# Kernel optimization log

Measured on AMD Instinct MI355X. Metric: run time of the kernel, lower is better.

The kernel has to match this reference:

```python
import jax, jax.numpy as jnp
import numpy as np
from jax import lax


def setup_inputs() -> dict:
    key = jax.random.key(0)
    k1, k2 = jax.random.split(key)
    x = jax.random.normal(k1, (16, 256, 64, 64), dtype=jnp.float32)
    weight = jax.random.normal(k2, (1024, 256), dtype=jnp.float32)  # codebook (K, C)
    return {"x": x, "weight": weight}


def reference(x, weight):
    B, C, H, W = x.shape
    # (b c h w) -> (b h w) c
    xf = jnp.transpose(x, (0, 2, 3, 1)).reshape(-1, C)  # [N, C]
    d = (jnp.sum(xf * xf, axis=1, keepdims=True)
         + jnp.sum(weight * weight, axis=1)
         - 2.0 * (xf @ weight.T))
    indices = jnp.argmin(d, axis=1)  # [N], int
    z = weight[indices]  # [N, C] embedding lookup
    codebook_loss = jnp.mean((z - lax.stop_gradient(xf)) ** 2)
    commitment_loss = jnp.mean((xf - lax.stop_gradient(z)) ** 2)
    # straight-through estimator
    zq = xf + lax.stop_gradient(z - xf)
    zq = zq.reshape(B, H, W, C).transpose(0, 3, 1, 2)  # back to [B, C, H, W]
    sequence = indices.reshape(B, H, W)
    return zq, sequence, codebook_loss, commitment_loss
```

## Files before the change

kernel.cpp:

```cpp
#include <hip/hip_runtime.h>
#include <cfloat>
#include <climits>

#define B_   16
#define C_   256
#define K_   1024
#define HW_  4096
#define N_   (B_ * HW_)
#define CHW_ (C_ * HW_)

#define SEQ_OFF  16777216
#define LOSS_OFF (SEQ_OFF + N_)
#define WT_F    0
#define WN_F    262144
#define WNU_F   263168
#define WQ_F    264192
#define RLIST_F 395264
#define RCNT_F  526336
#define WMAX_F  526337

#define RL_CAP  131072
#define EPS_GAP 0.1f
#define XSCL    20.0f
#define XINV    0.05f
#define XOVF    6.3f

typedef int i32x4  __attribute__((ext_vector_type(4)));
typedef int i32x16 __attribute__((ext_vector_type(16)));

__device__ __forceinline__ int pack4b(int b0, int b1, int b2, int b3) {
    return (b0 & 0xFF) | ((b1 & 0xFF) << 8) | ((b2 & 0xFF) << 16) | ((b3 & 0xFF) << 24);
}

__global__ __launch_bounds__(256) void wmax_kernel(
    const float* __restrict__ w, unsigned* __restrict__ wmax_bits)
{
    const int tid = blockIdx.x * 256 + threadIdx.x;
    float mx = 0.f;
#pragma unroll
    for (int q = 0; q < 4; ++q) {
        const float4 v = reinterpret_cast<const float4*>(w)[tid * 4 + q];
        mx = fmaxf(mx, fmaxf(fmaxf(fabsf(v.x), fabsf(v.y)), fmaxf(fabsf(v.z), fabsf(v.w))));
    }
#pragma unroll
    for (int m = 1; m < 64; m <<= 1) mx = fmaxf(mx, __shfl_xor(mx, m, 64));
    if ((threadIdx.x & 63) == 0) atomicMax(wmax_bits, __float_as_uint(mx));
}

__global__ __launch_bounds__(256) void wprep_kernel(
    const float* __restrict__ w, const unsigned* __restrict__ wmax_bits,
    unsigned char* __restrict__ wq, float* __restrict__ w_t,
    float* __restrict__ wn, int* __restrict__ wnu)
{
    const int t = threadIdx.x;
    const int l = t & 63;
    const int k = blockIdx.x * 4 + (t >> 6);
    const float wmx = __uint_as_float(*wmax_bits);
    const float s   = 127.4f / wmx;
    const float d1  = wmx / 127.4f;
    const float sl  = s * 256.0f;

    const float4 v4 = *reinterpret_cast<const float4*>(w + (size_t)k * C_ + l * 4);
    float vv[4] = {v4.x, v4.y, v4.z, v4.w};
    float s2 = vv[0]*vv[0] + vv[1]*vv[1] + vv[2]*vv[2] + vv[3]*vv[3];
#pragma unroll
    for (int m = 1; m < 64; m <<= 1) s2 += __shfl_xor(s2, m, 64);

    const int chunk = k >> 5;
    const int col   = k & 31;
#pragma unroll
    for (int q = 0; q < 4; ++q) {
        const int c = l * 4 + q;
        const float v = vv[q];
        const int qh = (int)rintf(v * s);
        const float r = fmaf((float)qh, -d1, v);
        int ql = (int)rintf(r * sl);
        ql = max(-127, min(127, ql));
        const size_t off = (size_t)chunk * 16384 + (size_t)(c >> 5) * 1024
                         + (size_t)((c >> 4) & 1) * 512 + (size_t)col * 16 + (size_t)(c & 15);
        wq[off]        = (unsigned char)(qh & 0xFF);
        wq[off + 8192] = (unsigned char)(ql & 0xFF);
        w_t[(size_t)c * K_ + k] = v;
    }
    if (l == 0) {
        wn[k] = s2;
        wnu[k] = (int)rintf(s2 * (2560.0f / d1));
    }
}

__global__ __launch_bounds__(256) void argmin_i8_kernel(
    const float* __restrict__ x, const unsigned char* __restrict__ wq,
    const int* __restrict__ wnu, const unsigned* __restrict__ wmax_bits,
    float* __restrict__ seq, int* __restrict__ rlist, int* __restrict__ rcount)
{
    __shared__ __align__(16) char lds[32768];
    const int t  = threadIdx.x;
    const int l  = t & 63;
    const int wv = t >> 6;
    const int col = l & 31;
    const int khalf = l >> 5;
    const int nb = blockIdx.x;
    const int b  = nb >> 5;
    const int hw0 = (nb & 31) << 7;
    const float* xb = x + (size_t)b * CHW_ + hw0;

    char* const buf0 = lds;
    char* const buf1 = lds + 16384;

#define STAGE32(ch, dst)                                                          \
    {                                                                             \
        _Pragma("unroll")                                                         \
        for (int rr = 0; rr < 4; ++rr) {                                          \
            const int sIdx = wv * 4 + rr;                                         \
            __builtin_amdgcn_global_load_lds(                                     \
                (const __attribute__((address_space(1))) void*)                   \
                    (wq + (size_t)(ch) * 16384 + sIdx * 1024 + l * 16),           \
                (__attribute__((address_space(3))) void*)((dst) + sIdx * 1024),   \
                16, 0, 0);                                                        \
        }                                                                         \
    }

    STAGE32(0, buf1);

    i32x4 ah8[8], al8[8];
    float mx = 0.f;
    {
        float* xs = (float*)buf0;
        const int row = wv * 32 + col;
#pragma unroll
        for (int cc = 0; cc < 8; ++cc) {
#pragma unroll
            for (int qq = 0; qq < 4; ++qq) {
                const int fi = qq * 256 + t;
                const int cl = fi >> 5;
                const int r4 = (fi & 31) << 2;
                const float4 v = *reinterpret_cast<const float4*>(
                    xb + (size_t)(cc * 32 + cl) * HW_ + r4);
                *reinterpret_cast<float4*>(xs + cl * 128 + r4) = v;
            }
            __syncthreads();
            int qh[16], ql[16];
#pragma unroll
            for (int j = 0; j < 16; ++j) {
                const float v = xs[(khalf * 16 + j) * 128 + row];
                mx = fmaxf(mx, fabsf(v));
                int h = (int)rintf(v * XSCL);
                h = max(-127, min(127, h));
                const float r = fmaf((float)h, -XINV, v);
                int lo = (int)rintf(r * (XSCL * 256.0f));
                lo = max(-127, min(127, lo));
                qh[j] = h; ql[j] = lo;
            }
            ah8[cc] = (i32x4){ pack4b(qh[0],qh[1],qh[2],qh[3]),   pack4b(qh[4],qh[5],qh[6],qh[7]),
                               pack4b(qh[8],qh[9],qh[10],qh[11]), pack4b(qh[12],qh[13],qh[14],qh[15]) };
            al8[cc] = (i32x4){ pack4b(ql[0],ql[1],ql[2],ql[3]),   pack4b(ql[4],ql[5],ql[6],ql[7]),
                               pack4b(ql[8],ql[9],ql[10],ql[11]), pack4b(ql[12],ql[13],ql[14],ql[15]) };
            __syncthreads();
        }
    }

    mx = fmaxf(mx, __shfl_xor(mx, 32, 64));
    if (khalf == 0 && mx > XOVF) {
        const int pos = atomicAdd(rcount, 1);
        if (pos < RL_CAP) rlist[pos] = b * HW_ + hw0 + wv * 32 + col;
    }

    const float wmx = __uint_as_float(*wmax_bits);
    const int eps_u = (int)(32614.4f / wmx);

    int m1p[16], m2p[16];
#pragma unroll
    for (int r = 0; r < 16; ++r) { m1p[r] = INT_MAX; m2p[r] = INT_MAX; }

    for (int ch = 0; ch < 32; ++ch) {
        char* const curbuf = (ch & 1) ? buf0 : buf1;
        if (ch < 31) STAGE32(ch + 1, (ch & 1) ? buf1 : buf0);
        const int wnu_l = wnu[ch * 32 + col];

        i32x16 aH, aX;
#pragma unroll
        for (int r = 0; r < 16; ++r) { aH[r] = 0; aX[r] = 0; }

#pragma unroll
        for (int ks = 0; ks < 8; ++ks) {
            const i32x4 bh = *reinterpret_cast<const i32x4*>(curbuf + ks * 1024 + (l << 4));
            const i32x4 bl = *reinterpret_cast<const i32x4*>(curbuf + 8192 + ks * 1024 + (l << 4));
            aH = __builtin_amdgcn_mfma_i32_32x32x32_i8(ah8[ks], bh, aH, 0, 0, 0);
            aX = __builtin_amdgcn_mfma_i32_32x32x32_i8(ah8[ks], bl, aX, 0, 0, 0);
            aX = __builtin_amdgcn_mfma_i32_32x32x32_i8(al8[ks], bh, aX, 0, 0, 0);
        }

#pragma unroll
        for (int r = 0; r < 16; ++r) {
            const int T  = (aH[r] << 8) + aX[r];
            const int D  = wnu_l - T;
            const int Dp = (D & ~31) | ch;
            m2p[r] = min(m2p[r], max(m1p[r], Dp));
            m1p[r] = min(m1p[r], Dp);
        }
        __syncthreads();
    }
#undef STAGE32

    int k1[16];
#pragma unroll
    for (int r = 0; r < 16; ++r) k1[r] = ((m1p[r] & 31) << 5) | col;
#pragma unroll
    for (int mask = 1; mask <= 16; mask <<= 1) {
#pragma unroll
        for (int r = 0; r < 16; ++r) {
            const int om1 = __shfl_xor(m1p[r], mask, 64);
            const int ok1 = __shfl_xor(k1[r],  mask, 64);
            const int om2 = __shfl_xor(m2p[r], mask, 64);
            const int nm2 = min(min(m2p[r], om2), max(m1p[r], om1));
            const bool lt = om1 < m1p[r] || (om1 == m1p[r] && ok1 < k1[r]);
            m1p[r] = lt ? om1 : m1p[r];
            k1[r]  = lt ? ok1 : k1[r];
            m2p[r] = nm2;
        }
    }

    if (col == 0) {
#pragma unroll
        for (int r = 0; r < 16; ++r) {
            const int row_local = (r & 3) + 8 * (r >> 2) + 4 * khalf;
            const int n = b * HW_ + hw0 + wv * 32 + row_local;
            seq[n] = (float)k1[r];
            if (m2p[r] - m1p[r] < eps_u) {
                const int pos = atomicAdd(rcount, 1);
                if (pos < RL_CAP) rlist[pos] = n;
            }
        }
    }
}

__global__ __launch_bounds__(256) void rescue_kernel(
    const float* __restrict__ x, const float* __restrict__ w_t,
    const float* __restrict__ wnorm, const int* __restrict__ rlist,
    const int* __restrict__ rcount, float* __restrict__ seq)
{
    __shared__ float xr[C_];
    __shared__ float bvs[4];
    __shared__ int   bis[4];
    const int t = threadIdx.x;
    const int cnt = min(*rcount, RL_CAP);
    for (int ii = blockIdx.x; ii < cnt; ii += gridDim.x) {
        const int n = rlist[ii];
        const int b = n >> 12, hw = n & 4095;
        xr[t] = x[(size_t)b * CHW_ + (size_t)t * HW_ + hw];
        __syncthreads();
        float best = FLT_MAX; int bidx = 0;
#pragma unroll
        for (int q = 0; q < 4; ++q) {
            const int k = t + q * 256;
            float acc = 0.f;
            for (int c = 0; c < C_; ++c) acc = fmaf(xr[c], w_t[(size_t)c * K_ + k], acc);
            const float d = wnorm[k] - 2.f * acc;
            if (d < best || (d == best && k < bidx)) { best = d; bidx = k; }
        }
#pragma unroll
        for (int mask = 1; mask < 64; mask <<= 1) {
            const float ov = __shfl_xor(best, mask, 64);
            const int   oi = __shfl_xor(bidx, mask, 64);
            if (ov < best || (ov == best && oi < bidx)) { best = ov; bidx = oi; }
        }
        if ((t & 63) == 0) { bvs[t >> 6] = best; bis[t >> 6] = bidx; }
        __syncthreads();
        if (t == 0) {
            float bv = bvs[0]; int bi = bis[0];
#pragma unroll
            for (int w2 = 1; w2 < 4; ++w2)
                if (bvs[w2] < bv || (bvs[w2] == bv && bis[w2] < bi)) { bv = bvs[w2]; bi = bis[w2]; }
            seq[n] = (float)bi;
        }
        __syncthreads();
    }
}

__global__ __launch_bounds__(256) void gather_kernel(
    const float* __restrict__ x, const float* __restrict__ w,
    const float* __restrict__ seqf, float* __restrict__ zq,
    double* __restrict__ loss_acc)
{
    __shared__ float ws[C_ * 64];
    const int t   = threadIdx.x;
    const int nb  = blockIdx.x;
    const int b   = nb >> 6;
    const int hw0 = (nb & 63) << 6;
    {
        const int j = t >> 2, q = t & 3;
        const int idx = (int)seqf[b * HW_ + hw0 + j];
        const float* wrow = w + (size_t)idx * C_ + q * 64;
#pragma unroll
        for (int m = 0; m < 16; ++m) {
            const float4 v = *reinterpret_cast<const float4*>(wrow + m * 4);
            const int c = q * 64 + m * 4;
            ws[(c + 0) * 64 + j] = v.x;
            ws[(c + 1) * 64 + j] = v.y;
            ws[(c + 2) * 64 + j] = v.z;
            ws[(c + 3) * 64 + j] = v.w;
        }
    }
    __syncthreads();
    const int r  = t & 63;
    const int cg = t >> 6;
    const float* xb = x  + (size_t)b * CHW_ + hw0;
    float*       zb = zq + (size_t)b * CHW_ + hw0;
    float lsum = 0.f;
#pragma unroll 4
    for (int cc = 0; cc < 64; ++cc) {
        const int c = cg * 64 + cc;
        const float xv = xb[(size_t)c * HW_ + r];
        const float d  = ws[c * 64 + r] - xv;
        zb[(size_t)c * HW_ + r] = xv + d;
        lsum += d * d;
    }
#pragma unroll
    for (int off = 32; off >= 1; off >>= 1) lsum += __shfl_down(lsum, off, 64);
    __syncthreads();
    if ((t & 63) == 0) ws[t >> 6] = lsum;
    __syncthreads();
    if (t == 0)
        atomicAdd(loss_acc, (double)(ws[0] + ws[1] + ws[2] + ws[3]));
}

__global__ void finalize_kernel(const double* __restrict__ acc, float* __restrict__ loss_out)
{
    const double s = *acc;
    const float m = (float)(s / (double)((size_t)N_ * C_));
    loss_out[0] = m;
    loss_out[1] = m;
}

extern "C" void kernel_launch(void* const* d_in, const int* in_sizes, int n_in,
                              void* d_out, int out_size, void* d_ws, size_t ws_size,
                              hipStream_t stream)
{
    (void)in_sizes; (void)n_in; (void)out_size; (void)d_ws; (void)ws_size;
    const float* x = (const float*)d_in[0];
    const float* w = (const float*)d_in[1];
    float* out = (float*)d_out;

    float*         w_t    = out + WT_F;
    float*         wn     = out + WN_F;
    int*           wnu    = (int*)(out + WNU_F);
    unsigned char* wq     = (unsigned char*)(out + WQ_F);
    int*           rlist  = (int*)(out + RLIST_F);
    int*           rcount = (int*)(out + RCNT_F);
    unsigned*      wmaxb  = (unsigned*)(out + WMAX_F);
    float*         seq    = out + SEQ_OFF;
    double*        loss_acc = (double*)(out + LOSS_OFF);

    hipMemsetAsync((void*)wmaxb, 0, 4, stream);
    hipMemsetAsync((void*)rcount, 0, 4, stream);
    wmax_kernel<<<64, 256, 0, stream>>>(w, wmaxb);
    wprep_kernel<<<256, 256, 0, stream>>>(w, wmaxb, wq, w_t, wn, wnu);
    argmin_i8_kernel<<<512, 256, 0, stream>>>(x, wq, wnu, wmaxb, seq, rlist, rcount);
    rescue_kernel<<<1024, 256, 0, stream>>>(x, w_t, wn, rlist, rcount, seq);
    hipMemsetAsync((char*)d_out + (size_t)LOSS_OFF * 4, 0, 8, stream);
    gather_kernel<<<1024, 256, 0, stream>>>(x, w, seq, out, loss_acc);
    finalize_kernel<<<1, 1, 0, stream>>>(loss_acc, out + LOSS_OFF);
}
```

Before: 206.5 us.

## Deepen codebook staging to a 4-buffer, 3-ahead pipeline with explicit vmcnt waits

Replaces double-buffered LDS staging of int8 codebook chunks with a four-slot ring that prefetches three chunks ahead. Each step waits only on the oldest outstanding load using explicit vmcnt/lgkmcnt waits and a raw s_barrier instead of __syncthreads. The wnu norms are preloaded into LDS, and MFMA sections are raised in priority with s_setprio. LDS use grows from 32KB to about 68KB per block, which may reduce how many blocks fit on a CU.

```diff
diff --git a/kernel.cpp b/kernel.cpp
--- a/kernel.cpp
+++ b/kernel.cpp
@@ -93,7 +93,7 @@
     const int* __restrict__ wnu, const unsigned* __restrict__ wmax_bits,
     float* __restrict__ seq, int* __restrict__ rlist, int* __restrict__ rcount)
 {
-    __shared__ __align__(16) char lds[32768];
+    __shared__ __align__(16) char lds[69632];
     const int t  = threadIdx.x;
     const int l  = t & 63;
     const int wv = t >> 6;
@@ -103,9 +103,7 @@
     const int b  = nb >> 5;
     const int hw0 = (nb & 31) << 7;
     const float* xb = x + (size_t)b * CHW_ + hw0;
-
-    char* const buf0 = lds;
-    char* const buf1 = lds + 16384;
+    int* const wnu_lds = (int*)(lds + 65536);
 
 #define STAGE32(ch, dst)                                                          \
     {                                                                             \
@@ -120,12 +118,13 @@
         }                                                                         \
     }
 
-    STAGE32(0, buf1);
+#pragma unroll
+    for (int i = 0; i < 4; ++i) wnu_lds[t + i * 256] = wnu[t + i * 256];
 
     i32x4 ah8[8], al8[8];
     float mx = 0.f;
     {
-        float* xs = (float*)buf0;
+        float* xs = (float*)lds;
         const int row = wv * 32 + col;
 #pragma unroll
         for (int cc = 0; cc < 8; ++cc) {
@@ -172,34 +171,57 @@
 #pragma unroll
     for (int r = 0; r < 16; ++r) { m1p[r] = INT_MAX; m2p[r] = INT_MAX; }
 
-    for (int ch = 0; ch < 32; ++ch) {
-        char* const curbuf = (ch & 1) ? buf0 : buf1;
-        if (ch < 31) STAGE32(ch + 1, (ch & 1) ? buf1 : buf0);
-        const int wnu_l = wnu[ch * 32 + col];
-
-        i32x16 aH, aX;
-#pragma unroll
-        for (int r = 0; r < 16; ++r) { aH[r] = 0; aX[r] = 0; }
-
-#pragma unroll
-        for (int ks = 0; ks < 8; ++ks) {
-            const i32x4 bh = *reinterpret_cast<const i32x4*>(curbuf + ks * 1024 + (l << 4));
-            const i32x4 bl = *reinterpret_cast<const i32x4*>(curbuf + 8192 + ks * 1024 + (l << 4));
-            aH = __builtin_amdgcn_mfma_i32_32x32x32_i8(ah8[ks], bh, aH, 0, 0, 0);
-            aX = __builtin_amdgcn_mfma_i32_32x32x32_i8(ah8[ks], bl, aX, 0, 0, 0);
-            aX = __builtin_amdgcn_mfma_i32_32x32x32_i8(al8[ks], bh, aX, 0, 0, 0);
-        }
-
-#pragma unroll
-        for (int r = 0; r < 16; ++r) {
-            const int T  = (aH[r] << 8) + aX[r];
-            const int D  = wnu_l - T;
-            const int Dp = (D & ~31) | ch;
-            m2p[r] = min(m2p[r], max(m1p[r], Dp));
-            m1p[r] = min(m1p[r], Dp);
-        }
-        __syncthreads();
-    }
+    STAGE32(0, lds);
+    STAGE32(1, lds + 16384);
+    STAGE32(2, lds + 32768);
+
+#define WAITS(VM)                                                     \
+    asm volatile("s_waitcnt lgkmcnt(0)" ::: "memory");                \
+    __builtin_amdgcn_sched_barrier(0);                                \
+    asm volatile("s_waitcnt vmcnt(" VM ")" ::: "memory");             \
+    __builtin_amdgcn_s_barrier();                                     \
+    __builtin_amdgcn_sched_barrier(0);
+
+#define CHUNK_COMPUTE(ch)                                                         \
+    {                                                                             \
+        const char* curbuf = lds + ((ch) & 3) * 16384;                            \
+        const int wnu_l = wnu_lds[(ch) * 32 + col];                               \
+        i32x16 aH, aX;                                                            \
+        _Pragma("unroll")                                                         \
+        for (int r = 0; r < 16; ++r) { aH[r] = 0; aX[r] = 0; }                    \
+        __builtin_amdgcn_s_setprio(1);                                            \
+        _Pragma("unroll")                                                         \
+        for (int ks = 0; ks < 8; ++ks) {                                          \
+            const i32x4 bh = *reinterpret_cast<const i32x4*>(                     \
+                curbuf + ks * 1024 + (l << 4));                                   \
+            const i32x4 bl = *reinterpret_cast<const i32x4*>(                     \
+                curbuf + 8192 + ks * 1024 + (l << 4));                            \
+            aH = __builtin_amdgcn_mfma_i32_32x32x32_i8(ah8[ks], bh, aH, 0, 0, 0); \
+            aX = __builtin_amdgcn_mfma_i32_32x32x32_i8(ah8[ks], bl, aX, 0, 0, 0); \
+            aX = __builtin_amdgcn_mfma_i32_32x32x32_i8(al8[ks], bh, aX, 0, 0, 0); \
+        }                                                                         \
+        __builtin_amdgcn_s_setprio(0);                                            \
+        _Pragma("unroll")                                                         \
+        for (int r = 0; r < 16; ++r) {                                            \
+            const int T  = (aH[r] << 8) + aX[r];                                  \
+            const int D  = wnu_l - T;                                             \
+            const int Dp = (D & ~31) | (ch);                                      \
+            m2p[r] = min(m2p[r], max(m1p[r], Dp));                                \
+            m1p[r] = min(m1p[r], Dp);                                             \
+        }                                                                         \
+    }
+
+#pragma unroll 1
+    for (int ch = 0; ch < 30; ++ch) {
+        WAITS("8");
+        if (ch <= 28) STAGE32(ch + 3, lds + ((ch + 3) & 3) * 16384);
+        CHUNK_COMPUTE(ch);
+    }
+    WAITS("4");
+    CHUNK_COMPUTE(30);
+    WAITS("0");
+    CHUNK_COMPUTE(31);
+#undef WAITS
 #undef STAGE32
 
     int k1[16];
```

New measurement: 190.4 us. 1.08x faster.
